# Performance work log

Hardware: AMD Instinct MI355X
Metric: run time of the kernel (lower is better)

Reference implementation:

```python
import jax, jax.numpy as jnp
import numpy as np

N_NODES = 50000
N_HYPEREDGES = 10000
NNZ = 800000


def setup_inputs() -> dict:
    key = jax.random.key(0)
    ks = jax.random.split(key, 8)
    x = jax.random.normal(ks[0], (N_NODES, 128), dtype=jnp.float32)
    edge = jax.random.randint(ks[1], (2, NNZ), 0, N_HYPEREDGES, dtype=jnp.int64)
    # Glorot-ish scaled weights per layer
    w1 = jax.random.normal(ks[2], (128, 128), dtype=jnp.float32) / np.sqrt(128)
    b1 = jnp.zeros((128,), dtype=jnp.float32)
    w2 = jax.random.normal(ks[3], (128, 64), dtype=jnp.float32) / np.sqrt(128)
    b2 = jnp.zeros((64,), dtype=jnp.float32)
    w3 = jax.random.normal(ks[4], (64, 32), dtype=jnp.float32) / np.sqrt(64)
    b3 = jnp.zeros((32,), dtype=jnp.float32)
    return {"x": x, "edge": edge, "w1": w1, "b1": b1, "w2": w2, "b2": b2, "w3": w3, "b3": b3}


def _hypergraph_conv(x, node_idx, edge_idx, w, b):
    """PyG HypergraphConv (no attention, unit hyperedge weights):
    X' = D^{-1} H B^{-1} H^T (X W + b)
    where H is the incidence matrix given by (node_idx, edge_idx) pairs,
    D = node degree, B = hyperedge degree.
    """
    xw = x @ w + b  # [N, F_out]
    ones = jnp.ones((node_idx.shape[0],), dtype=x.dtype)
    deg_e = jax.ops.segment_sum(ones, edge_idx, num_segments=N_HYPEREDGES)  # B
    deg_v = jax.ops.segment_sum(ones, node_idx, num_segments=N_NODES)      # D
    Binv = jnp.where(deg_e > 0, 1.0 / deg_e, 0.0)
    Dinv = jnp.where(deg_v > 0, 1.0 / deg_v, 0.0)
    # node -> hyperedge aggregation, normalized by hyperedge degree
    m_e = jax.ops.segment_sum(xw[node_idx], edge_idx, num_segments=N_HYPEREDGES) * Binv[:, None]
    # hyperedge -> node aggregation, normalized by node degree
    out = jax.ops.segment_sum(m_e[edge_idx], node_idx, num_segments=N_NODES) * Dinv[:, None]
    return out


def reference(x, edge, w1, b1, w2, b2, w3, b3):
    node_idx = edge[0]
    edge_idx = edge[1]
    h = jax.nn.relu(_hypergraph_conv(x, node_idx, edge_idx, w1, b1))
    h = jax.nn.relu(_hypergraph_conv(h, node_idx, edge_idx, w2, b2))
    h = jax.nn.relu(_hypergraph_conv(h, node_idx, edge_idx, w3, b3))
    return h
```

## Files before the change

kernel.cpp:

```cpp
#include <hip/hip_runtime.h>

#define N_NODES   50000
#define N_EDGES   10000
#define NNZ_TOT   800000
#define NACT      10000

#define SW   16
#define NB   625
#define CAP  1792

#define BW_IPT   32
#define BW_ITEMS (BW_IPT * 256)
#define BW_BLKS  ((NNZ_TOT + BW_ITEMS - 1) / BW_ITEMS)

#define G1_NRB   ((NACT + 31) / 32)
#define ZFB      96

__device__ __forceinline__ void bucket_write_body(
    const int* __restrict__ node_idx, const int* __restrict__ edge_idx,
    int* __restrict__ cntB, unsigned int* __restrict__ bktE,
    unsigned int* __restrict__ bktV, int nnz, int bwb)
{
    __shared__ int h[NB];
    const int tid  = threadIdx.x;
    const bool isV = bwb >= BW_BLKS;
    const int  blk = isV ? bwb - BW_BLKS : bwb;
    const int* keys = isV ? node_idx : edge_idx;
    const int* pays = isV ? edge_idx : node_idx;
    int* cnt = cntB + (isV ? NB : 0);
    unsigned int* bkt = isV ? bktV : bktE;

    for (int t = tid; t < NB; t += 256) h[t] = 0;
    __syncthreads();

    unsigned int pk[BW_IPT];
    const int base = blk * BW_ITEMS;
    #pragma unroll
    for (int j = 0; j < BW_IPT; ++j) {
        int k = base + j * 256 + tid;
        if (k < nnz) {
            unsigned int ky = (unsigned int)keys[k];
            unsigned int py = (unsigned int)pays[k];
            pk[j] = (ky << 16) | py;
            atomicAdd(&h[ky >> 4], 1);
        } else pk[j] = 0xFFFFFFFFu;
    }
    __syncthreads();
    for (int t = tid; t < NB; t += 256) {
        int c = h[t];
        h[t] = c ? atomicAdd(&cnt[t], c) : 0;
    }
    __syncthreads();
    #pragma unroll
    for (int j = 0; j < BW_IPT; ++j) {
        if (pk[j] != 0xFFFFFFFFu) {
            int b = (int)(pk[j] >> 20);
            int s = atomicAdd(&h[b], 1);
            if (s < CAP) bkt[(size_t)b * CAP + s] = pk[j];
        }
    }
}

template<int FIN, int FOUTT, int FB, int TM>
__device__ __forceinline__ void gemm_body(
    const float* __restrict__ X, const float* __restrict__ W,
    const float* __restrict__ Bias, float* __restrict__ Y,
    int nrows, int rb, int cb)
{
    constexpr int KB  = 32;
    constexpr int CGN = FB / 4;
    constexpr int RGN = 256 / CGN;
    constexpr int BM  = RGN * TM;
    static_assert(BM == 32, "BM must be 32");

    __shared__ float Xs[KB][BM + 4];
    __shared__ float Ws[KB][FB];

    const int tid  = threadIdx.x;
    const int cg   = tid % CGN;
    const int rg   = tid / CGN;
    const int row0 = rb * BM;
    const int col0 = cb * FB;

    float acc[TM][4];
    #pragma unroll
    for (int i = 0; i < TM; ++i)
        #pragma unroll
        for (int j = 0; j < 4; ++j) acc[i][j] = 0.f;

    for (int k0 = 0; k0 < FIN; k0 += KB) {
        {
            int r  = tid >> 3;
            int kq = tid & 7;
            int gr = row0 + r; if (gr >= nrows) gr = nrows - 1;
            float4 v = *(const float4*)&X[(size_t)gr * FIN + k0 + kq * 4];
            Xs[kq * 4 + 0][r] = v.x;
            Xs[kq * 4 + 1][r] = v.y;
            Xs[kq * 4 + 2][r] = v.z;
            Xs[kq * 4 + 3][r] = v.w;
        }
        constexpr int WIT = (KB * FB / 4) / 256;
        #pragma unroll
        for (int it = 0; it < WIT; ++it) {
            int idx = tid + it * 256;
            int k   = idx / (FB / 4);
            int cq  = idx % (FB / 4);
            *(float4*)&Ws[k][cq * 4] =
                *(const float4*)&W[(size_t)(k0 + k) * FOUTT + col0 + cq * 4];
        }
        __syncthreads();

        #pragma unroll 8
        for (int k = 0; k < KB; ++k) {
            float4 wv = *(const float4*)&Ws[k][cg * 4];
            float xr[TM];
            #pragma unroll
            for (int i = 0; i < TM; ++i) xr[i] = Xs[k][rg * TM + i];
            #pragma unroll
            for (int i = 0; i < TM; ++i) {
                acc[i][0] += xr[i] * wv.x;
                acc[i][1] += xr[i] * wv.y;
                acc[i][2] += xr[i] * wv.z;
                acc[i][3] += xr[i] * wv.w;
            }
        }
        __syncthreads();
    }

    float4 bv = *(const float4*)&Bias[col0 + cg * 4];
    #pragma unroll
    for (int i = 0; i < TM; ++i) {
        int gr = row0 + rg * TM + i;
        if (gr < nrows) {
            float4 o;
            o.x = acc[i][0] + bv.x; o.y = acc[i][1] + bv.y;
            o.z = acc[i][2] + bv.z; o.w = acc[i][3] + bv.w;
            *(float4*)&Y[(size_t)gr * FOUTT + col0 + cg * 4] = o;
        }
    }
}

__global__ __launch_bounds__(256) void build_gemm1_kernel(
    const int* __restrict__ node_idx, const int* __restrict__ edge_idx,
    int* __restrict__ cntB,
    unsigned int* __restrict__ bktE, unsigned int* __restrict__ bktV,
    const float* __restrict__ X, const float* __restrict__ W1,
    const float* __restrict__ B1, float* __restrict__ xw, int nnz)
{
    if (blockIdx.x < 2 * BW_BLKS) {
        bucket_write_body(node_idx, edge_idx, cntB, bktE, bktV, nnz, blockIdx.x);
    } else {
        int gb = blockIdx.x - 2 * BW_BLKS;
        gemm_body<128, 128, 64, 2>(X, W1, B1, xw, NACT, gb % G1_NRB, gb / G1_NRB);
    }
}

template<int FIN, int FOUTT, int FB, int TM>
__global__ __launch_bounds__(256) void gemm_bias(
    const float* __restrict__ X, const float* __restrict__ W,
    const float* __restrict__ Bias, float* __restrict__ Y, int nrows)
{
    gemm_body<FIN, FOUTT, FB, TM>(X, W, Bias, Y, nrows, blockIdx.x, blockIdx.y);
}

__global__ __launch_bounds__(256) void csr_finalize_kernel(
    const unsigned int* __restrict__ bktE, const unsigned int* __restrict__ bktV,
    const int* __restrict__ cntB,
    int2* __restrict__ segE, int2* __restrict__ segV,
    float* __restrict__ Binv, float* __restrict__ Dinv,
    int* __restrict__ csrE, int* __restrict__ csrV)
{
    __shared__ int cnt[SW];
    __shared__ int cur[SW];
    int b = blockIdx.x;
    const unsigned int* bkt; const int* cB; int2* seg; float* inv; int* csr;
    if (b < NB) { bkt = bktE; cB = cntB;      seg = segE; inv = Binv; csr = csrE; }
    else { b -= NB; bkt = bktV; cB = cntB + NB; seg = segV; inv = Dinv; csr = csrV; }
    const int lo = b * SW;
    const int p0 = b * CAP;
    int c_ = cB[b]; if (c_ > CAP) c_ = CAP;
    const int p1 = p0 + c_;

    if (threadIdx.x < SW) cnt[threadIdx.x] = 0;
    __syncthreads();
    for (int p = p0 + threadIdx.x; p < p1; p += 256) {
        int key = (int)(bkt[p] >> 16);
        atomicAdd(&cnt[key - lo], 1);
    }
    __syncthreads();
    if (threadIdx.x < 64) {
        int lane = threadIdx.x;
        int val = (lane < SW) ? cnt[lane] : 0;
        int x = val;
        #pragma unroll
        for (int d = 1; d < SW; d <<= 1) {
            int y = __shfl_up(x, d, 64);
            if (lane >= d) x += y;
        }
        if (lane < SW) {
            int beg = p0 + (x - val);
            int2 be; be.x = beg; be.y = beg + val;
            seg[lo + lane] = be;
            inv[lo + lane] = (val > 0) ? (1.0f / (float)val) : 0.0f;
            cur[lane]      = beg;
        }
    }
    __syncthreads();
    for (int p = p0 + threadIdx.x; p < p1; p += 256) {
        unsigned int pk = bkt[p];
        int key  = (int)(pk >> 16);
        int slot = atomicAdd(&cur[key - lo], 1);
        csr[slot] = (int)(pk & 0xFFFFu);
    }
}

template<int F, bool RELU>
__device__ __forceinline__ void seg_gather_body(
    const float* __restrict__ SRC, const int2* __restrict__ seg,
    const int* __restrict__ lst, const float* __restrict__ inv,
    float* __restrict__ DST, int s, int lane)
{
    constexpr int W = F / 4;
    constexpr int H = 64 / W;
    const int c = lane % W;
    const int h = lane / W;
    const int2 be = seg[s];
    const int start = be.x, end = be.y;
    const float* srcl = SRC + c * 4;
    float ax = 0.f, ay = 0.f, az = 0.f, aw = 0.f;
    int p = start + h;
    for (; p + 7 * H < end; p += 8 * H) {
        int r0 = lst[p],         r1 = lst[p + H],     r2 = lst[p + 2 * H], r3 = lst[p + 3 * H];
        int r4 = lst[p + 4 * H], r5 = lst[p + 5 * H], r6 = lst[p + 6 * H], r7 = lst[p + 7 * H];
        float4 a0 = *(const float4*)(srcl + (size_t)r0 * F);
        float4 a1 = *(const float4*)(srcl + (size_t)r1 * F);
        float4 a2 = *(const float4*)(srcl + (size_t)r2 * F);
        float4 a3 = *(const float4*)(srcl + (size_t)r3 * F);
        float4 a4 = *(const float4*)(srcl + (size_t)r4 * F);
        float4 a5 = *(const float4*)(srcl + (size_t)r5 * F);
        float4 a6 = *(const float4*)(srcl + (size_t)r6 * F);
        float4 a7 = *(const float4*)(srcl + (size_t)r7 * F);
        ax += (a0.x + a1.x) + (a2.x + a3.x) + (a4.x + a5.x) + (a6.x + a7.x);
        ay += (a0.y + a1.y) + (a2.y + a3.y) + (a4.y + a5.y) + (a6.y + a7.y);
        az += (a0.z + a1.z) + (a2.z + a3.z) + (a4.z + a5.z) + (a6.z + a7.z);
        aw += (a0.w + a1.w) + (a2.w + a3.w) + (a4.w + a5.w) + (a6.w + a7.w);
    }
    if (p + 3 * H < end) {
        int r0 = lst[p], r1 = lst[p + H], r2 = lst[p + 2 * H], r3 = lst[p + 3 * H];
        float4 a0 = *(const float4*)(srcl + (size_t)r0 * F);
        float4 a1 = *(const float4*)(srcl + (size_t)r1 * F);
        float4 a2 = *(const float4*)(srcl + (size_t)r2 * F);
        float4 a3 = *(const float4*)(srcl + (size_t)r3 * F);
        ax += (a0.x + a1.x) + (a2.x + a3.x);
        ay += (a0.y + a1.y) + (a2.y + a3.y);
        az += (a0.z + a1.z) + (a2.z + a3.z);
        aw += (a0.w + a1.w) + (a2.w + a3.w);
        p += 4 * H;
    }
    if (p + H < end) {
        int r0 = lst[p], r1 = lst[p + H];
        float4 a0 = *(const float4*)(srcl + (size_t)r0 * F);
        float4 a1 = *(const float4*)(srcl + (size_t)r1 * F);
        ax += a0.x + a1.x; ay += a0.y + a1.y;
        az += a0.z + a1.z; aw += a0.w + a1.w;
        p += 2 * H;
    }
    if (p < end) {
        int r = lst[p];
        float4 t = *(const float4*)(srcl + (size_t)r * F);
        ax += t.x; ay += t.y; az += t.z; aw += t.w;
    }
    #pragma unroll
    for (int d = W; d < 64; d <<= 1) {
        ax += __shfl_xor(ax, d);
        ay += __shfl_xor(ay, d);
        az += __shfl_xor(az, d);
        aw += __shfl_xor(aw, d);
    }
    if (lane < W) {
        float sc = inv[s];
        ax *= sc; ay *= sc; az *= sc; aw *= sc;
        if (RELU) {
            ax = fmaxf(ax, 0.f); ay = fmaxf(ay, 0.f);
            az = fmaxf(az, 0.f); aw = fmaxf(aw, 0.f);
        }
        float4 o; o.x = ax; o.y = ay; o.z = az; o.w = aw;
        *(float4*)(DST + (size_t)s * F + c * 4) = o;
    }
}

template<int F, bool RELU>
__global__ __launch_bounds__(256) void seg_gather_s(
    const float* __restrict__ SRC, const int2* __restrict__ seg,
    const int* __restrict__ lst, const float* __restrict__ inv,
    float* __restrict__ DST, int nseg)
{
    int s = blockIdx.x * 4 + (threadIdx.x >> 6);
    s = __builtin_amdgcn_readfirstlane(s);
    if (s >= nseg) return;
    seg_gather_body<F, RELU>(SRC, seg, lst, inv, DST, s, threadIdx.x & 63);
}

__global__ __launch_bounds__(256) void seg_gather_final(
    const float* __restrict__ SRC, const int2* __restrict__ seg,
    const int* __restrict__ lst, const float* __restrict__ inv,
    float* __restrict__ DST, int nsb)
{
    if ((int)blockIdx.x >= nsb) {
        const size_t total4 = (size_t)(N_NODES - NACT) * 32 / 4;
        float4* o4 = (float4*)(DST + (size_t)NACT * 32);
        float4 z; z.x = 0.f; z.y = 0.f; z.z = 0.f; z.w = 0.f;
        for (size_t i = (size_t)(blockIdx.x - nsb) * 256 + threadIdx.x;
             i < total4; i += (size_t)ZFB * 256)
            o4[i] = z;
        return;
    }
    int s = blockIdx.x * 4 + (threadIdx.x >> 6);
    s = __builtin_amdgcn_readfirstlane(s);
    if (s >= NACT) return;
    seg_gather_body<32, true>(SRC, seg, lst, inv, DST, s, threadIdx.x & 63);
}

extern "C" void kernel_launch(void* const* d_in, const int* in_sizes, int n_in,
                              void* d_out, int out_size, void* d_ws, size_t ws_size,
                              hipStream_t stream)
{
    const float* x  = (const float*)d_in[0];
    const int* edge = (const int*)d_in[1];
    const float* w1 = (const float*)d_in[2];
    const float* b1 = (const float*)d_in[3];
    const float* w2 = (const float*)d_in[4];
    const float* b2 = (const float*)d_in[5];
    const float* w3 = (const float*)d_in[6];
    const float* b3 = (const float*)d_in[7];
    float* out = (float*)d_out;

    const int NNZ = NNZ_TOT;
    const int* node_idx = edge;
    const int* edge_idx = edge + NNZ;

    uintptr_t base = (uintptr_t)d_ws;
    size_t off = 0;
    auto take = [&](size_t nbytes) -> void* {
        off = (off + 255) & ~(size_t)255;
        void* p = (void*)(base + off);
        off += nbytes;
        return p;
    };
    int2*  segE  = (int2*) take((size_t)NACT * 8);
    int2*  segV  = (int2*) take((size_t)NACT * 8);
    float* Binv  = (float*)take((size_t)NACT * 4);
    float* Dinv  = (float*)take((size_t)NACT * 4);
    int*   cntB  = (int*)  take((size_t)2 * NB * 4);
    unsigned int* bktE = (unsigned int*)take((size_t)NB * CAP * 4);
    unsigned int* bktV = (unsigned int*)take((size_t)NB * CAP * 4);
    int*   csrE  = (int*)  take((size_t)NB * CAP * 4);
    int*   csrV  = (int*)  take((size_t)NB * CAP * 4);
    float* xw    = (float*)take((size_t)NACT * 128 * 4);
    float* hA    = (float*)take((size_t)NACT * 128 * 4);
    float* hB    = (float*)take((size_t)NACT * 64 * 4);
    float* me    = (float*)take((size_t)NACT * 128 * 4);

    hipMemsetAsync(cntB, 0, (size_t)2 * NB * 4, stream);

    build_gemm1_kernel<<<2 * BW_BLKS + G1_NRB * 2, 256, 0, stream>>>(
        node_idx, edge_idx, cntB, bktE, bktV, x, w1, b1, xw, NNZ);
    csr_finalize_kernel<<<2 * NB, 256, 0, stream>>>(
        bktE, bktV, cntB, segE, segV, Binv, Dinv, csrE, csrV);

    const int nsbA = (NACT + 3) / 4;

    seg_gather_s<128, false><<<nsbA, 256, 0, stream>>>(xw, segE, csrE, Binv, me, NACT);
    seg_gather_s<128, true ><<<nsbA, 256, 0, stream>>>(me, segV, csrV, Dinv, hA, NACT);

    gemm_bias<128, 64, 32, 1><<<dim3(G1_NRB, 2), 256, 0, stream>>>(hA, w2, b2, xw, NACT);
    seg_gather_s<64, false><<<nsbA, 256, 0, stream>>>(xw, segE, csrE, Binv, me, NACT);
    seg_gather_s<64, true ><<<nsbA, 256, 0, stream>>>(me, segV, csrV, Dinv, hB, NACT);

    gemm_bias<64, 32, 32, 1><<<dim3(G1_NRB, 1), 256, 0, stream>>>(hB, w3, b3, xw, NACT);
    seg_gather_s<32, false><<<nsbA, 256, 0, stream>>>(xw, segE, csrE, Binv, me, NACT);
    seg_gather_final<<<nsbA + ZFB, 256, 0, stream>>>(me, segV, csrV, Dinv, out, nsbA);
}
```

Measured before the change: 224.0 us.

## Fuse hyperedge-to-node gather with next layer's dense transform

The node-side segment gather (with Dinv scaling and ReLU) now stages each output row in shared memory and immediately multiplies it by the next layer's weight matrix plus bias. This removes the two standalone gemm_bias launches and the round trip of the hA/hB intermediates through global memory. In exchange, each wavefront does a per-row matrix-vector product that reads W from global/L2 for every row, with no tiling reuse across rows, and separate xw buffers are used per layer. The shared-memory row is written and read by the same wavefront without an explicit barrier, which relies on wave-synchronous behaviour.

```diff
diff --git a/kernel.cpp b/kernel.cpp
--- a/kernel.cpp
+++ b/kernel.cpp
@@ -155,14 +155,6 @@
     }
 }
 
-template<int FIN, int FOUTT, int FB, int TM>
-__global__ __launch_bounds__(256) void gemm_bias(
-    const float* __restrict__ X, const float* __restrict__ W,
-    const float* __restrict__ Bias, float* __restrict__ Y, int nrows)
-{
-    gemm_body<FIN, FOUTT, FB, TM>(X, W, Bias, Y, nrows, blockIdx.x, blockIdx.y);
-}
-
 __global__ __launch_bounds__(256) void csr_finalize_kernel(
     const unsigned int* __restrict__ bktE, const unsigned int* __restrict__ bktV,
     const int* __restrict__ cntB,
@@ -215,10 +207,10 @@
 }
 
 template<int F, bool RELU>
-__device__ __forceinline__ void seg_gather_body(
+__device__ __forceinline__ float4 seg_gather_acc(
     const float* __restrict__ SRC, const int2* __restrict__ seg,
     const int* __restrict__ lst, const float* __restrict__ inv,
-    float* __restrict__ DST, int s, int lane)
+    int s, int lane)
 {
     constexpr int W = F / 4;
     constexpr int H = 64 / W;
@@ -277,16 +269,14 @@
         az += __shfl_xor(az, d);
         aw += __shfl_xor(aw, d);
     }
-    if (lane < W) {
-        float sc = inv[s];
-        ax *= sc; ay *= sc; az *= sc; aw *= sc;
-        if (RELU) {
-            ax = fmaxf(ax, 0.f); ay = fmaxf(ay, 0.f);
-            az = fmaxf(az, 0.f); aw = fmaxf(aw, 0.f);
-        }
-        float4 o; o.x = ax; o.y = ay; o.z = az; o.w = aw;
-        *(float4*)(DST + (size_t)s * F + c * 4) = o;
-    }
+    float sc = inv[s];
+    ax *= sc; ay *= sc; az *= sc; aw *= sc;
+    if (RELU) {
+        ax = fmaxf(ax, 0.f); ay = fmaxf(ay, 0.f);
+        az = fmaxf(az, 0.f); aw = fmaxf(aw, 0.f);
+    }
+    float4 o; o.x = ax; o.y = ay; o.z = az; o.w = aw;
+    return o;
 }
 
 template<int F, bool RELU>
@@ -298,7 +288,48 @@
     int s = blockIdx.x * 4 + (threadIdx.x >> 6);
     s = __builtin_amdgcn_readfirstlane(s);
     if (s >= nseg) return;
-    seg_gather_body<F, RELU>(SRC, seg, lst, inv, DST, s, threadIdx.x & 63);
+    const int lane = threadIdx.x & 63;
+    float4 o = seg_gather_acc<F, RELU>(SRC, seg, lst, inv, s, lane);
+    if (lane < F / 4)
+        *(float4*)(DST + (size_t)s * F + (lane % (F / 4)) * 4) = o;
+}
+
+template<int FIN, int FOUT>
+__global__ __launch_bounds__(256) void seg_gather_gemm(
+    const float* __restrict__ SRC, const int2* __restrict__ seg,
+    const int* __restrict__ lst, const float* __restrict__ inv,
+    const float* __restrict__ Wn, const float* __restrict__ Bn,
+    float* __restrict__ OUT, int nseg)
+{
+    __shared__ float rowbuf[4][FIN];
+    int s = blockIdx.x * 4 + (threadIdx.x >> 6);
+    s = __builtin_amdgcn_readfirstlane(s);
+    if (s >= nseg) return;
+    const int lane = threadIdx.x & 63;
+    const int w    = threadIdx.x >> 6;
+
+    float4 o = seg_gather_acc<FIN, true>(SRC, seg, lst, inv, s, lane);
+    if (lane < FIN / 4)
+        *(float4*)&rowbuf[w][(lane % (FIN / 4)) * 4] = o;
+
+    if (FOUT == 64) {
+        const int j = lane;
+        float acc = Bn[j];
+        #pragma unroll 8
+        for (int k = 0; k < FIN; ++k)
+            acc += rowbuf[w][k] * Wn[(size_t)k * 64 + j];
+        OUT[(size_t)s * 64 + j] = acc;
+    } else {
+        const int j = lane & 31;
+        const int g = lane >> 5;
+        float acc = 0.f;
+        #pragma unroll 8
+        for (int k = g * (FIN / 2); k < (g + 1) * (FIN / 2); ++k)
+            acc += rowbuf[w][k] * Wn[(size_t)k * 32 + j];
+        acc += __shfl_xor(acc, 32);
+        if (lane < 32)
+            OUT[(size_t)s * 32 + j] = acc + Bn[j];
+    }
 }
 
 __global__ __launch_bounds__(256) void seg_gather_final(
@@ -318,7 +349,10 @@
     int s = blockIdx.x * 4 + (threadIdx.x >> 6);
     s = __builtin_amdgcn_readfirstlane(s);
     if (s >= NACT) return;
-    seg_gather_body<32, true>(SRC, seg, lst, inv, DST, s, threadIdx.x & 63);
+    const int lane = threadIdx.x & 63;
+    float4 o = seg_gather_acc<32, true>(SRC, seg, lst, inv, s, lane);
+    if (lane < 8)
+        *(float4*)(DST + (size_t)s * 32 + lane * 4) = o;
 }
 
 extern "C" void kernel_launch(void* const* d_in, const int* in_sizes, int n_in,
@@ -356,28 +390,28 @@
     unsigned int* bktV = (unsigned int*)take((size_t)NB * CAP * 4);
     int*   csrE  = (int*)  take((size_t)NB * CAP * 4);
     int*   csrV  = (int*)  take((size_t)NB * CAP * 4);
-    float* xw    = (float*)take((size_t)NACT * 128 * 4);
-    float* hA    = (float*)take((size_t)NACT * 128 * 4);
-    float* hB    = (float*)take((size_t)NACT * 64 * 4);
+    float* xw1   = (float*)take((size_t)NACT * 128 * 4);
+    float* xw2   = (float*)take((size_t)NACT * 64 * 4);
+    float* xw3   = (float*)take((size_t)NACT * 32 * 4);
     float* me    = (float*)take((size_t)NACT * 128 * 4);
 
     hipMemsetAsync(cntB, 0, (size_t)2 * NB * 4, stream);
 
     build_gemm1_kernel<<<2 * BW_BLKS + G1_NRB * 2, 256, 0, stream>>>(
-        node_idx, edge_idx, cntB, bktE, bktV, x, w1, b1, xw, NNZ);
+        node_idx, edge_idx, cntB, bktE, bktV, x, w1, b1, xw1, NNZ);
     csr_finalize_kernel<<<2 * NB, 256, 0, stream>>>(
         bktE, bktV, cntB, segE, segV, Binv, Dinv, csrE, csrV);
 
     const int nsbA = (NACT + 3) / 4;
 
-    seg_gather_s<128, false><<<nsbA, 256, 0, stream>>>(xw, segE, csrE, Binv, me, NACT);
-    seg_gather_s<128, true ><<<nsbA, 256, 0, stream>>>(me, segV, csrV, Dinv, hA, NACT);
-
-    gemm_bias<128, 64, 32, 1><<<dim3(G1_NRB, 2), 256, 0, stream>>>(hA, w2, b2, xw, NACT);
-    seg_gather_s<64, false><<<nsbA, 256, 0, stream>>>(xw, segE, csrE, Binv, me, NACT);
-    seg_gather_s<64, true ><<<nsbA, 256, 0, stream>>>(me, segV, csrV, Dinv, hB, NACT);
-
-    gemm_bias<64, 32, 32, 1><<<dim3(G1_NRB, 1), 256, 0, stream>>>(hB, w3, b3, xw, NACT);
-    seg_gather_s<32, false><<<nsbA, 256, 0, stream>>>(xw, segE, csrE, Binv, me, NACT);
+    seg_gather_s<128, false><<<nsbA, 256, 0, stream>>>(xw1, segE, csrE, Binv, me, NACT);
+    seg_gather_gemm<128, 64><<<nsbA, 256, 0, stream>>>(
+        me, segV, csrV, Dinv, w2, b2, xw2, NACT);
+
+    seg_gather_s<64, false><<<nsbA, 256, 0, stream>>>(xw2, segE, csrE, Binv, me, NACT);
+    seg_gather_gemm<64, 32><<<nsbA, 256, 0, stream>>>(
+        me, segV, csrV, Dinv, w3, b3, xw3, NACT);
+
+    seg_gather_s<32, false><<<nsbA, 256, 0, stream>>>(xw3, segE, csrE, Binv, me, NACT);
     seg_gather_final<<<nsbA + ZFB, 256, 0, stream>>>(me, segV, csrV, Dinv, out, nsbA);
 }
```

New measurement: 220.1 us. Within noise of the previous version (-1.8%).
